# Kernel tuning notes

Measured on AMD Instinct MI355X. Metric: run time of the kernel, lower is better.

Reference implementation:

```python
import jax, jax.numpy as jnp
import numpy as np

N_STEPS = 2   # n_steps; n_head = 1 (module is only consistent for a single head)
NEG_SLOPE = 0.2


def setup_inputs() -> dict:
    key = jax.random.key(0)
    ks = jax.random.split(key, 6)
    B, C, N = 8, 2048, 2048  # N must equal input_dim (coefs*out broadcast requirement)
    s = 1.0 / np.sqrt(C).astype(np.float32)
    x = jax.random.normal(ks[0], (B, C, N), jnp.float32)
    Wa = jax.random.normal(ks[1], (C, C), jnp.float32) * s   # conv1x1, no bias
    Wb = jax.random.normal(ks[2], (C,), jnp.float32) * s     # conv1x1 -> 1 channel
    bb = jnp.zeros((1,), jnp.float32)
    Wc = jax.random.normal(ks[3], (C,), jnp.float32) * s
    bc = jnp.zeros((1,), jnp.float32)
    bias = jnp.zeros((C,), jnp.float32)                      # self.bias (zeros)
    return dict(x=x, Wa=Wa, Wb=Wb, bb=bb, Wc=Wc, bc=bc, bias=bias)


def _head_attention(out, Wa, Wb, bb, Wc, bc, bias):
    # dropout p=0.0 -> identity
    h = jnp.einsum('oc,bcn->bon', Wa, out)            # [B,C,N] conv1x1 projection
    t1 = jnp.einsum('c,bcn->bn', Wb, h) + bb          # [B,N]
    t2 = jnp.einsum('c,bcn->bn', Wc, h) + bc          # [B,N]
    z = t1[:, None, :] + t2[:, :, None]               # [B,N,N] additive outer-sum
    z = jnp.where(z >= 0, z, NEG_SLOPE * z)           # leaky_relu(0.2)
    # torch F.softmax with no dim on a 3D tensor uses legacy dim=0 (batch dim)
    coefs = jax.nn.softmax(z, axis=0)
    re = coefs * h + bias                             # bias broadcasts over last axis
    return re                                         # [B,N,N] (== [B,C,N] since N==C)


def reference(x, Wa, Wb, bb, Wc, bc, bias):
    out = x
    for _ in range(N_STEPS):
        # n_head == 1: stack of one head then mean is the head itself
        out = _head_attention(out, Wa, Wb, bb, Wc, bc, bias)
    return out
```

## Files before the change

### kernel.cpp

```cpp
#include <hip/hip_runtime.h>
#include <hip/hip_bf16.h>

typedef unsigned short ushort_t;
typedef __attribute__((ext_vector_type(8))) short bf16x8;
typedef __attribute__((ext_vector_type(4))) float f32x4;
typedef __attribute__((ext_vector_type(8))) unsigned short u16x8;
typedef __attribute__((ext_vector_type(4))) unsigned short u16x4;

#define NDIM 2048
#define BDIM 8

__device__ __forceinline__ float bf2f(unsigned short u) {
  union { unsigned int i; float f; } v; v.i = ((unsigned int)u) << 16; return v.f;
}
__device__ __forceinline__ unsigned short f2bf(float f) {
  union { float f; unsigned int i; } v; v.f = f;
  unsigned int x = v.i;
  x += 0x7fffu + ((x >> 16) & 1u);
  return (unsigned short)(x >> 16);
}

__device__ __forceinline__ void gload16(const void* g, void* l) {
  __builtin_amdgcn_global_load_lds(
      (const __attribute__((address_space(1))) void*)g,
      (__attribute__((address_space(3))) void*)l,
      16, 0, 0);
}

__global__ __launch_bounds__(256) void pack_a(const float* __restrict__ Wa,
                                              unsigned short* __restrict__ Apk) {
  const int sub = blockIdx.x * 4 + (threadIdx.x >> 6);
  const int l   = threadIdx.x & 63;
  const int mt  = sub >> 6, kt = sub & 63;
  const int fr  = l & 15, fs = l >> 4;
  const float* src = Wa + (size_t)(mt * 16 + fr) * NDIM + kt * 32 + fs * 8;
  f32x4 v0 = *(const f32x4*)&src[0];
  f32x4 v1 = *(const f32x4*)&src[4];
  u16x8 w;
  #pragma unroll
  for (int k = 0; k < 4; ++k) { w[k] = f2bf(v0[k]); w[4 + k] = f2bf(v1[k]); }
  *(u16x8*)&Apk[(size_t)sub * 512 + l * 8] = w;
}

__global__ __launch_bounds__(256) void transpose_convert(const float* __restrict__ x,
                                                         unsigned short* __restrict__ dst) {
  __shared__ float tile[64][65];
  const int b  = blockIdx.z;
  const int n0 = blockIdx.x * 64;
  const int c0 = blockIdx.y * 64;
  const int tr = threadIdx.x >> 4;
  const int tc = threadIdx.x & 15;
  const float* src = x + ((size_t)b * NDIM + c0) * NDIM + n0;
  #pragma unroll
  for (int p = 0; p < 4; ++p) {
    int r = p * 16 + tr;
    f32x4 v = *(const f32x4*)&src[(size_t)r * NDIM + tc * 4];
    #pragma unroll
    for (int k = 0; k < 4; ++k) tile[r][tc * 4 + k] = v[k];
  }
  __syncthreads();
  unsigned short* d = dst + ((size_t)b * NDIM + n0) * NDIM + c0;
  #pragma unroll
  for (int p = 0; p < 4; ++p) {
    int r = p * 16 + tr;
    u16x4 w;
    #pragma unroll
    for (int k = 0; k < 4; ++k) w[k] = f2bf(tile[tc * 4 + k][r]);
    *(u16x4*)&d[(size_t)r * NDIM + tc * 4] = w;
  }
}

__global__ __launch_bounds__(256) void weff1(const float* __restrict__ Wa,
                                             const float* __restrict__ Wb,
                                             const float* __restrict__ Wc,
                                             float* __restrict__ part) {
  int c  = blockIdx.x * 256 + threadIdx.x;
  int o0 = blockIdx.y * 128;
  float ab = 0.f, ac = 0.f;
  for (int o = o0; o < o0 + 128; ++o) {
    float w = Wa[(size_t)o * NDIM + c];
    ab = fmaf(Wb[o], w, ab);
    ac = fmaf(Wc[o], w, ac);
  }
  part[(size_t)(blockIdx.y * 2 + 0) * NDIM + c] = ab;
  part[(size_t)(blockIdx.y * 2 + 1) * NDIM + c] = ac;
}
__global__ __launch_bounds__(256) void weff2(const float* __restrict__ part,
                                             float* __restrict__ wbe, float* __restrict__ wce) {
  int c = blockIdx.x * 256 + threadIdx.x;
  float ab = 0.f, ac = 0.f;
  #pragma unroll
  for (int i = 0; i < 16; ++i) {
    ab += part[(size_t)(i * 2 + 0) * NDIM + c];
    ac += part[(size_t)(i * 2 + 1) * NDIM + c];
  }
  wbe[c] = ab; wce[c] = ac;
}

__global__ __launch_bounds__(256) void t_kernel(const unsigned short* __restrict__ curT,
                                                const float* __restrict__ wbe,
                                                const float* __restrict__ wce,
                                                const float* __restrict__ bb,
                                                const float* __restrict__ bc,
                                                float* __restrict__ t1, float* __restrict__ t2) {
  int row  = blockIdx.x * 4 + (threadIdx.x >> 6);
  int lane = threadIdx.x & 63;
  const unsigned short* r = curT + (size_t)row * NDIM;
  float a1 = 0.f, a2 = 0.f;
  #pragma unroll
  for (int p = 0; p < 4; ++p) {
    int c0 = p * 512 + lane * 8;
    u16x8 v = *(const u16x8*)&r[c0];
    f32x4 w1a = *(const f32x4*)&wbe[c0];
    f32x4 w1b = *(const f32x4*)&wbe[c0 + 4];
    f32x4 w2a = *(const f32x4*)&wce[c0];
    f32x4 w2b = *(const f32x4*)&wce[c0 + 4];
    #pragma unroll
    for (int j = 0; j < 4; ++j) {
      float xv = bf2f(v[j]);
      a1 = fmaf(w1a[j], xv, a1);
      a2 = fmaf(w2a[j], xv, a2);
    }
    #pragma unroll
    for (int j = 0; j < 4; ++j) {
      float xv = bf2f(v[4 + j]);
      a1 = fmaf(w1b[j], xv, a1);
      a2 = fmaf(w2b[j], xv, a2);
    }
  }
  #pragma unroll
  for (int off = 32; off > 0; off >>= 1) {
    a1 += __shfl_xor(a1, off);
    a2 += __shfl_xor(a2, off);
  }
  if (lane == 0) { t1[row] = a1 + bb[0]; t2[row] = a2 + bc[0]; }
}

__global__ __launch_bounds__(256) void s_kernel(const float* __restrict__ t1,
                                                const float* __restrict__ t2,
                                                float* __restrict__ S) {
  int n = blockIdx.x * 256 + threadIdx.x;
  int o = blockIdx.y;
  float acc = 0.f;
  #pragma unroll
  for (int b = 0; b < BDIM; ++b) {
    float z = t1[b * NDIM + n] + t2[b * NDIM + o];
    z = z >= 0.f ? z : 0.2f * z;
    acc += __expf(z);
  }
  S[(size_t)o * NDIM + n] = __logf(acc);
}

__global__ __launch_bounds__(512, 2) void gemm_fused(
    const unsigned short* __restrict__ Apk,
    const unsigned short* __restrict__ Bt,
    const float* __restrict__ t1, const float* __restrict__ t2,
    const float* __restrict__ S,  const float* __restrict__ bias,
    unsigned short* __restrict__ outT,
    float* __restrict__ outF,
    int write_f32) {
  __shared__ __align__(16) unsigned short sbuf[2][16384];

  const int tid  = threadIdx.x;
  const int lane = tid & 63;
  const int w    = tid >> 6;
  const int wr   = w >> 2;
  const int wc   = w & 3;
  const int bn0  = blockIdx.x * 256;
  const int bm0  = blockIdx.y * 256;
  const int bz   = blockIdx.z;
  const unsigned short* Bb = Bt + (size_t)bz * NDIM * NDIM;

  f32x4 acc[8][4];
  #pragma unroll
  for (int m = 0; m < 8; ++m)
    #pragma unroll
    for (int n = 0; n < 4; ++n) acc[m][n] = (f32x4){0.f, 0.f, 0.f, 0.f};

  const int sst   = (lane & 7) ^ (lane >> 3);
  const int srowl = lane >> 3;
  const unsigned short* bG = Bb + (size_t)(bn0 + w * 32 + srowl) * NDIM + sst * 8;
  auto stB = [&](int T, int p, int d) {
    gload16(bG + (size_t)p * 8 * NDIM + T * 64, &sbuf[d][(w * 32 + p * 8) * 64]);
  };

  const int fr  = lane & 15;
  const int fs  = lane >> 4;
  const int sl0 = ((fs) ^ (fr & 7)) * 8;
  const int sl1 = ((4 + fs) ^ (fr & 7)) * 8;
  const int bRow = (wc * 64 + fr) * 64;

  const unsigned int mtBase = (unsigned)((bm0 >> 4) + wr * 8);
  unsigned int aOff0[4], aOff1[4];
  #pragma unroll
  for (int m = 0; m < 4; ++m) {
    aOff0[m] = ((mtBase + m) * 64u) * 1024u + lane * 16u;
    aOff1[m] = ((mtBase + 4 + m) * 64u) * 1024u + lane * 16u;
  }

  bf16x8 Am0[4][2], Am1[4][2], bv[2][2];

  auto issueA = [&](bf16x8 (&dst)[4][2], const unsigned int (&off)[4]) {
    #pragma unroll
    for (int m = 0; m < 4; ++m) {
      asm volatile("global_load_dwordx4 %0, %1, %2"
                   : "=v"(dst[m][0]) : "v"(off[m]), "s"(Apk) : "memory");
      asm volatile("global_load_dwordx4 %0, %1, %2 offset:1024"
                   : "=v"(dst[m][1]) : "v"(off[m]), "s"(Apk) : "memory");
    }
  };
  auto rdB = [&](int nh, int d) {
    #pragma unroll
    for (int n = 0; n < 2; ++n) {
      const int base = d * 16384 + bRow + (nh * 2 + n) * 16 * 64;
      bv[n][0] = *(const bf16x8*)&sbuf[0][base + sl0];
      bv[n][1] = *(const bf16x8*)&sbuf[0][base + sl1];
    }
  };
  auto quad = [&](bf16x8 (&af)[4][2], int mo, int no) {
    __builtin_amdgcn_s_setprio(1);
    #pragma unroll
    for (int m = 0; m < 4; ++m)
      #pragma unroll
      for (int n = 0; n < 2; ++n)
        #pragma unroll
        for (int ks = 0; ks < 2; ++ks)
          acc[mo + m][no + n] = __builtin_amdgcn_mfma_f32_16x16x32_bf16(
              af[m][ks], bv[n][ks], acc[mo + m][no + n], 0, 0, 0);
    __builtin_amdgcn_s_setprio(0);
    __builtin_amdgcn_sched_barrier(0);
  };

  stB(0, 0, 0); stB(0, 1, 0); stB(0, 2, 0); stB(0, 3, 0);
  issueA(Am0, aOff0);
  asm volatile("s_waitcnt vmcnt(8)" ::: "memory");
  __builtin_amdgcn_s_barrier();

  #pragma clang loop unroll(disable)
  for (int tt = 0; tt < 16; ++tt) {
    const int Tn0 = 2 * tt + 1;
    const int Tn1 = (tt == 15) ? 31 : 2 * tt + 2;

    #pragma unroll
    for (int half = 0; half < 2; ++half) {
      const int cur = half, nxt = half ^ 1;
      const int Tn = half ? Tn1 : Tn0;

      issueA(Am1, aOff1);
      #pragma unroll
      for (int m = 0; m < 4; ++m) aOff1[m] += 2048u;
      rdB(0, cur);
      asm volatile("s_waitcnt vmcnt(8)" ::: "memory");
      __builtin_amdgcn_sched_barrier(0);
      quad(Am0, 0, 0);

      stB(Tn, 0, nxt); stB(Tn, 1, nxt);
      asm volatile("s_waitcnt vmcnt(2)" ::: "memory");
      __builtin_amdgcn_sched_barrier(0);
      quad(Am1, 4, 0);

      stB(Tn, 2, nxt); stB(Tn, 3, nxt);
      rdB(1, cur);
      #pragma unroll
      for (int m = 0; m < 4; ++m) aOff0[m] += 2048u;
      __builtin_amdgcn_sched_barrier(0);
      quad(Am0, 0, 2);

      issueA(Am0, aOff0);
      __builtin_amdgcn_sched_barrier(0);
      quad(Am1, 4, 2);

      asm volatile("s_waitcnt vmcnt(8)" ::: "memory");
      __builtin_amdgcn_s_barrier();
    }
  }

  asm volatile("s_waitcnt vmcnt(0)" ::: "memory");
  __syncthreads();

  float* sT1f = (float*)&sbuf[0][0];
  float* sT2f = sT1f + 256;
  if (tid < 256) sT1f[tid] = t1[bz * NDIM + bn0 + tid];
  else           sT2f[tid - 256] = t2[bz * NDIM + bm0 + (tid - 256)];
  __syncthreads();

  const int lr4 = fs * 4;
  #pragma unroll
  for (int m = 0; m < 8; ++m) {
    #pragma unroll
    for (int n = 0; n < 4; ++n) {
      const int oo = wr * 128 + m * 16 + lr4;
      const int nn = wc * 64 + n * 16 + fr;
      const int o  = bm0 + oo;
      const int ng = bn0 + nn;
      const float tz1  = sT1f[nn];
      const float bval = bias[ng];
      if (write_f32) {
        #pragma unroll
        for (int r = 0; r < 4; ++r) {
          float z = tz1 + sT2f[oo + r];
          z = z >= 0.f ? z : 0.2f * z;
          float coef = __expf(z - S[(size_t)(o + r) * NDIM + ng]);
          outF[(size_t)bz * NDIM * NDIM + (size_t)(o + r) * NDIM + ng] =
              fmaf(coef, acc[m][n][r], bval);
        }
      } else {
        u16x4 wv;
        #pragma unroll
        for (int r = 0; r < 4; ++r) {
          float z = tz1 + sT2f[oo + r];
          z = z >= 0.f ? z : 0.2f * z;
          float coef = __expf(z - S[(size_t)(o + r) * NDIM + ng]);
          wv[r] = f2bf(fmaf(coef, acc[m][n][r], bval));
        }
        *(u16x4*)&outT[(size_t)bz * NDIM * NDIM + (size_t)ng * NDIM + o] = wv;
      }
    }
  }
}

extern "C" void kernel_launch(void* const* d_in, const int* in_sizes, int n_in,
                              void* d_out, int out_size, void* d_ws, size_t ws_size,
                              hipStream_t stream) {
  const float* x    = (const float*)d_in[0];
  const float* Wa   = (const float*)d_in[1];
  const float* Wb   = (const float*)d_in[2];
  const float* bb   = (const float*)d_in[3];
  const float* Wc   = (const float*)d_in[4];
  const float* bc   = (const float*)d_in[5];
  const float* bias = (const float*)d_in[6];
  float* out = (float*)d_out;

  char* ws = (char*)d_ws;
  unsigned short* curA = (unsigned short*)ws; ws += (size_t)BDIM * NDIM * NDIM * 2;
  unsigned short* curB = (unsigned short*)ws; ws += (size_t)BDIM * NDIM * NDIM * 2;
  unsigned short* Apk  = (unsigned short*)ws; ws += (size_t)NDIM * NDIM * 2;
  float* t1   = (float*)ws; ws += (size_t)BDIM * NDIM * 4;
  float* t2   = (float*)ws; ws += (size_t)BDIM * NDIM * 4;
  float* wbe  = (float*)ws; ws += NDIM * 4;
  float* wce  = (float*)ws; ws += NDIM * 4;
  float* part = (float*)ws; ws += (size_t)32 * NDIM * 4;
  float* S    = (float*)ws; ws += (size_t)NDIM * NDIM * 4;

  pack_a<<<2048, 256, 0, stream>>>(Wa, Apk);
  transpose_convert<<<dim3(32, 32, BDIM), 256, 0, stream>>>(x, curA);
  weff1<<<dim3(8, 16), 256, 0, stream>>>(Wa, Wb, Wc, part);
  weff2<<<8, 256, 0, stream>>>(part, wbe, wce);

  for (int step = 0; step < 2; ++step) {
    const unsigned short* cur = step ? curB : curA;
    t_kernel<<<(BDIM * NDIM) / 4, 256, 0, stream>>>(cur, wbe, wce, bb, bc, t1, t2);
    s_kernel<<<dim3(NDIM / 256, NDIM), 256, 0, stream>>>(t1, t2, S);
    gemm_fused<<<dim3(8, 8, BDIM), 512, 0, stream>>>(
        Apk, cur, t1, t2, S, bias, curB, out, step);
  }
}
```

Baseline: 375.9 us.

## Fuse t1/t2 projections into transpose and GEMM epilogue via atomics

Removes the separate t_kernel pass, which re-read the full bf16 activation tensor at each step. t1/t2 are now built as partial dot products inside transpose_convert, and for step 2 inside the step-1 GEMM epilogue, then reduced with shuffles and accumulated with global atomicAdd into zeroed buffers. The bb/bc biases move into s_kernel and the GEMM epilogue. The price is extra epilogue FMAs, atomics, memsets and double-buffered t arrays, and the float sums become nondeterministic. The dot product now uses fp32 values rather than bf16-rounded ones.

```diff
diff --git a/kernel.cpp b/kernel.cpp
--- a/kernel.cpp
+++ b/kernel.cpp
@@ -42,8 +42,10 @@
   *(u16x8*)&Apk[(size_t)sub * 512 + l * 8] = w;
 }
 
-__global__ __launch_bounds__(256) void transpose_convert(const float* __restrict__ x,
-                                                         unsigned short* __restrict__ dst) {
+__global__ __launch_bounds__(256) void transpose_convert(
+    const float* __restrict__ x, unsigned short* __restrict__ dst,
+    const float* __restrict__ wbe, const float* __restrict__ wce,
+    float* __restrict__ t1, float* __restrict__ t2) {
   __shared__ float tile[64][65];
   const int b  = blockIdx.z;
   const int n0 = blockIdx.x * 64;
@@ -59,14 +61,34 @@
     for (int k = 0; k < 4; ++k) tile[r][tc * 4 + k] = v[k];
   }
   __syncthreads();
+  float w1[4], w2[4];
+  #pragma unroll
+  for (int k = 0; k < 4; ++k) {
+    w1[k] = wbe[c0 + tc * 4 + k];
+    w2[k] = wce[c0 + tc * 4 + k];
+  }
   unsigned short* d = dst + ((size_t)b * NDIM + n0) * NDIM + c0;
   #pragma unroll
   for (int p = 0; p < 4; ++p) {
     int r = p * 16 + tr;
     u16x4 w;
-    #pragma unroll
-    for (int k = 0; k < 4; ++k) w[k] = f2bf(tile[tc * 4 + k][r]);
+    float a1 = 0.f, a2 = 0.f;
+    #pragma unroll
+    for (int k = 0; k < 4; ++k) {
+      float v = tile[tc * 4 + k][r];
+      w[k] = f2bf(v);
+      a1 = fmaf(w1[k], v, a1);
+      a2 = fmaf(w2[k], v, a2);
+    }
     *(u16x4*)&d[(size_t)r * NDIM + tc * 4] = w;
+    a1 += __shfl_xor(a1, 1); a1 += __shfl_xor(a1, 2);
+    a1 += __shfl_xor(a1, 4); a1 += __shfl_xor(a1, 8);
+    a2 += __shfl_xor(a2, 1); a2 += __shfl_xor(a2, 2);
+    a2 += __shfl_xor(a2, 4); a2 += __shfl_xor(a2, 8);
+    if (tc == 0) {
+      atomicAdd(&t1[(size_t)b * NDIM + n0 + r], a1);
+      atomicAdd(&t2[(size_t)b * NDIM + n0 + r], a2);
+    }
   }
 }
 
@@ -97,54 +119,18 @@
   wbe[c] = ab; wce[c] = ac;
 }
 
-__global__ __launch_bounds__(256) void t_kernel(const unsigned short* __restrict__ curT,
-                                                const float* __restrict__ wbe,
-                                                const float* __restrict__ wce,
+__global__ __launch_bounds__(256) void s_kernel(const float* __restrict__ t1,
+                                                const float* __restrict__ t2,
                                                 const float* __restrict__ bb,
                                                 const float* __restrict__ bc,
-                                                float* __restrict__ t1, float* __restrict__ t2) {
-  int row  = blockIdx.x * 4 + (threadIdx.x >> 6);
-  int lane = threadIdx.x & 63;
-  const unsigned short* r = curT + (size_t)row * NDIM;
-  float a1 = 0.f, a2 = 0.f;
-  #pragma unroll
-  for (int p = 0; p < 4; ++p) {
-    int c0 = p * 512 + lane * 8;
-    u16x8 v = *(const u16x8*)&r[c0];
-    f32x4 w1a = *(const f32x4*)&wbe[c0];
-    f32x4 w1b = *(const f32x4*)&wbe[c0 + 4];
-    f32x4 w2a = *(const f32x4*)&wce[c0];
-    f32x4 w2b = *(const f32x4*)&wce[c0 + 4];
-    #pragma unroll
-    for (int j = 0; j < 4; ++j) {
-      float xv = bf2f(v[j]);
-      a1 = fmaf(w1a[j], xv, a1);
-      a2 = fmaf(w2a[j], xv, a2);
-    }
-    #pragma unroll
-    for (int j = 0; j < 4; ++j) {
-      float xv = bf2f(v[4 + j]);
-      a1 = fmaf(w1b[j], xv, a1);
-      a2 = fmaf(w2b[j], xv, a2);
-    }
-  }
-  #pragma unroll
-  for (int off = 32; off > 0; off >>= 1) {
-    a1 += __shfl_xor(a1, off);
-    a2 += __shfl_xor(a2, off);
-  }
-  if (lane == 0) { t1[row] = a1 + bb[0]; t2[row] = a2 + bc[0]; }
-}
-
-__global__ __launch_bounds__(256) void s_kernel(const float* __restrict__ t1,
-                                                const float* __restrict__ t2,
                                                 float* __restrict__ S) {
   int n = blockIdx.x * 256 + threadIdx.x;
   int o = blockIdx.y;
+  const float bias2 = bb[0] + bc[0];
   float acc = 0.f;
   #pragma unroll
   for (int b = 0; b < BDIM; ++b) {
-    float z = t1[b * NDIM + n] + t2[b * NDIM + o];
+    float z = t1[b * NDIM + n] + t2[b * NDIM + o] + bias2;
     z = z >= 0.f ? z : 0.2f * z;
     acc += __expf(z);
   }
@@ -155,7 +141,10 @@
     const unsigned short* __restrict__ Apk,
     const unsigned short* __restrict__ Bt,
     const float* __restrict__ t1, const float* __restrict__ t2,
+    const float* __restrict__ bb, const float* __restrict__ bc,
     const float* __restrict__ S,  const float* __restrict__ bias,
+    const float* __restrict__ wbe, const float* __restrict__ wce,
+    float* __restrict__ t1o, float* __restrict__ t2o,
     unsigned short* __restrict__ outT,
     float* __restrict__ outF,
     int write_f32) {
@@ -280,22 +269,22 @@
 
   float* sT1f = (float*)&sbuf[0][0];
   float* sT2f = sT1f + 256;
-  if (tid < 256) sT1f[tid] = t1[bz * NDIM + bn0 + tid];
-  else           sT2f[tid - 256] = t2[bz * NDIM + bm0 + (tid - 256)];
+  if (tid < 256) sT1f[tid] = t1[bz * NDIM + bn0 + tid] + bb[0];
+  else           sT2f[tid - 256] = t2[bz * NDIM + bm0 + (tid - 256)] + bc[0];
   __syncthreads();
 
   const int lr4 = fs * 4;
-  #pragma unroll
-  for (int m = 0; m < 8; ++m) {
-    #pragma unroll
-    for (int n = 0; n < 4; ++n) {
+  if (write_f32) {
+    #pragma unroll
+    for (int m = 0; m < 8; ++m) {
       const int oo = wr * 128 + m * 16 + lr4;
-      const int nn = wc * 64 + n * 16 + fr;
       const int o  = bm0 + oo;
-      const int ng = bn0 + nn;
-      const float tz1  = sT1f[nn];
-      const float bval = bias[ng];
-      if (write_f32) {
+      #pragma unroll
+      for (int n = 0; n < 4; ++n) {
+        const int nn = wc * 64 + n * 16 + fr;
+        const int ng = bn0 + nn;
+        const float tz1  = sT1f[nn];
+        const float bval = bias[ng];
         #pragma unroll
         for (int r = 0; r < 4; ++r) {
           float z = tz1 + sT2f[oo + r];
@@ -304,16 +293,46 @@
           outF[(size_t)bz * NDIM * NDIM + (size_t)(o + r) * NDIM + ng] =
               fmaf(coef, acc[m][n][r], bval);
         }
-      } else {
+      }
+    }
+  } else {
+    float tp1[4] = {0.f, 0.f, 0.f, 0.f}, tp2[4] = {0.f, 0.f, 0.f, 0.f};
+    #pragma unroll
+    for (int m = 0; m < 8; ++m) {
+      const int oo = wr * 128 + m * 16 + lr4;
+      const int o  = bm0 + oo;
+      float w1[4], w2[4];
+      #pragma unroll
+      for (int r = 0; r < 4; ++r) { w1[r] = wbe[o + r]; w2[r] = wce[o + r]; }
+      #pragma unroll
+      for (int n = 0; n < 4; ++n) {
+        const int nn = wc * 64 + n * 16 + fr;
+        const int ng = bn0 + nn;
+        const float tz1  = sT1f[nn];
+        const float bval = bias[ng];
         u16x4 wv;
         #pragma unroll
         for (int r = 0; r < 4; ++r) {
           float z = tz1 + sT2f[oo + r];
           z = z >= 0.f ? z : 0.2f * z;
           float coef = __expf(z - S[(size_t)(o + r) * NDIM + ng]);
-          wv[r] = f2bf(fmaf(coef, acc[m][n][r], bval));
+          float val  = fmaf(coef, acc[m][n][r], bval);
+          wv[r] = f2bf(val);
+          tp1[n] = fmaf(w1[r], val, tp1[n]);
+          tp2[n] = fmaf(w2[r], val, tp2[n]);
         }
         *(u16x4*)&outT[(size_t)bz * NDIM * NDIM + (size_t)ng * NDIM + o] = wv;
+      }
+    }
+    #pragma unroll
+    for (int n = 0; n < 4; ++n) {
+      float a1 = tp1[n], a2 = tp2[n];
+      a1 += __shfl_xor(a1, 16); a1 += __shfl_xor(a1, 32);
+      a2 += __shfl_xor(a2, 16); a2 += __shfl_xor(a2, 32);
+      if (fs == 0) {
+        const int ng = bn0 + wc * 64 + n * 16 + fr;
+        atomicAdd(&t1o[(size_t)bz * NDIM + ng], a1);
+        atomicAdd(&t2o[(size_t)bz * NDIM + ng], a2);
       }
     }
   }
@@ -335,23 +354,30 @@
   unsigned short* curA = (unsigned short*)ws; ws += (size_t)BDIM * NDIM * NDIM * 2;
   unsigned short* curB = (unsigned short*)ws; ws += (size_t)BDIM * NDIM * NDIM * 2;
   unsigned short* Apk  = (unsigned short*)ws; ws += (size_t)NDIM * NDIM * 2;
-  float* t1   = (float*)ws; ws += (size_t)BDIM * NDIM * 4;
-  float* t2   = (float*)ws; ws += (size_t)BDIM * NDIM * 4;
+  float* t1a  = (float*)ws; ws += (size_t)BDIM * NDIM * 4;
+  float* t2a  = (float*)ws; ws += (size_t)BDIM * NDIM * 4;
+  float* t1b  = (float*)ws; ws += (size_t)BDIM * NDIM * 4;
+  float* t2b  = (float*)ws; ws += (size_t)BDIM * NDIM * 4;
   float* wbe  = (float*)ws; ws += NDIM * 4;
   float* wce  = (float*)ws; ws += NDIM * 4;
   float* part = (float*)ws; ws += (size_t)32 * NDIM * 4;
   float* S    = (float*)ws; ws += (size_t)NDIM * NDIM * 4;
 
+  hipMemsetAsync(t1a, 0, (size_t)BDIM * NDIM * 4, stream);
+  hipMemsetAsync(t2a, 0, (size_t)BDIM * NDIM * 4, stream);
+  hipMemsetAsync(t1b, 0, (size_t)BDIM * NDIM * 4, stream);
+  hipMemsetAsync(t2b, 0, (size_t)BDIM * NDIM * 4, stream);
+
   pack_a<<<2048, 256, 0, stream>>>(Wa, Apk);
-  transpose_convert<<<dim3(32, 32, BDIM), 256, 0, stream>>>(x, curA);
   weff1<<<dim3(8, 16), 256, 0, stream>>>(Wa, Wb, Wc, part);
   weff2<<<8, 256, 0, stream>>>(part, wbe, wce);
-
-  for (int step = 0; step < 2; ++step) {
-    const unsigned short* cur = step ? curB : curA;
-    t_kernel<<<(BDIM * NDIM) / 4, 256, 0, stream>>>(cur, wbe, wce, bb, bc, t1, t2);
-    s_kernel<<<dim3(NDIM / 256, NDIM), 256, 0, stream>>>(t1, t2, S);
-    gemm_fused<<<dim3(8, 8, BDIM), 512, 0, stream>>>(
-        Apk, cur, t1, t2, S, bias, curB, out, step);
-  }
-}
+  transpose_convert<<<dim3(32, 32, BDIM), 256, 0, stream>>>(x, curA, wbe, wce, t1a, t2a);
+
+  s_kernel<<<dim3(NDIM / 256, NDIM), 256, 0, stream>>>(t1a, t2a, bb, bc, S);
+  gemm_fused<<<dim3(8, 8, BDIM), 512, 0, stream>>>(
+      Apk, curA, t1a, t2a, bb, bc, S, bias, wbe, wce, t1b, t2b, curB, out, 0);
+
+  s_kernel<<<dim3(NDIM / 256, NDIM), 256, 0, stream>>>(t1b, t2b, bb, bc, S);
+  gemm_fused<<<dim3(8, 8, BDIM), 512, 0, stream>>>(
+      Apk, curB, t1b, t2b, bb, bc, S, bias, wbe, wce, t1a, t2a, curB, out, 1);
+}
```

After: 367.0 us. 1.02x faster.
